# Optimization experiments

Measured on AMD Instinct MI355X. Metric: run time of the kernel, lower is better.

The kernel has to match this reference:

```python
import jax, jax.numpy as jnp
import numpy as np

L_MAX = 16      # max phrase span length in tokens
MARGIN = 0.4    # CosineEmbeddingLoss margin
EPS = 1e-8


def _span_max_pool(sent_emb, sid, start, length):
    """Vectorized ragged span max-pooling.
    sent_emb: [B, S, D]; sid/start/length: [N] int. length in [0, L_MAX-1],
    actual span length = length + 1 (spans are non-empty).
    Returns [N, D].
    """
    offs = jnp.arange(L_MAX, dtype=start.dtype)                  # [L]
    pos = start[:, None] + offs[None, :]                          # [N, L]
    mask = offs[None, :] <= length[:, None]                       # [N, L] (len+1 valid)
    vals = sent_emb[sid[:, None], pos]                            # [N, L, D] gather
    vals = jnp.where(mask[:, :, None], vals, -jnp.inf)
    return jnp.max(vals, axis=1)                                  # [N, D]


def setup_inputs() -> dict:
    key = jax.random.key(0)
    ks = jax.random.split(key, 7)
    B, S, D, N = 64, 512, 1024, 8192
    sent_emb = jax.random.normal(ks[0], (B, S, D), dtype=jnp.float32)
    sid = jax.random.randint(ks[1], (N,), 0, B, dtype=jnp.int32)
    s_start = jax.random.randint(ks[2], (N,), 0, S - L_MAX, dtype=jnp.int32)
    s_len = jax.random.randint(ks[3], (N,), 0, L_MAX, dtype=jnp.int32)
    t_start = jax.random.randint(ks[4], (N,), 0, S - L_MAX, dtype=jnp.int32)
    t_len = jax.random.randint(ks[5], (N,), 0, L_MAX, dtype=jnp.int32)
    labels = jax.random.randint(ks[6], (N,), 0, 2, dtype=jnp.int32)
    return {"sent_emb": sent_emb, "sid": sid, "s_start": s_start, "s_len": s_len,
            "t_start": t_start, "t_len": t_len, "labels": labels}


def reference(sent_emb, sid, s_start, s_len, t_start, t_len, labels):
    # Ragged span max-pooling for source and target phrases
    s_emb = _span_max_pool(sent_emb, sid, s_start, s_len)   # [N, D]
    t_emb = _span_max_pool(sent_emb, sid, t_start, t_len)   # [N, D]
    # CosineEmbeddingLoss (mean reduction), y in {-1, +1}
    dot = jnp.sum(s_emb * t_emb, axis=-1)
    cos = dot / (jnp.linalg.norm(s_emb, axis=-1) * jnp.linalg.norm(t_emb, axis=-1) + EPS)
    y = 2.0 * labels.astype(cos.dtype) - 1.0
    per_pair = jnp.where(y > 0, 1.0 - cos, jnp.maximum(0.0, cos - MARGIN))
    return jnp.mean(per_pair)
```

## Files before the change

### kernel.cpp

```cpp
#include <hip/hip_runtime.h>

#define L_MAX 16
#define MARGIN 0.4f
#define EPS 1e-8f

__global__ __launch_bounds__(256) void span_pair_loss_kernel(
    const float* __restrict__ emb,
    const int*   __restrict__ sid,
    const int*   __restrict__ s_start,
    const int*   __restrict__ s_len,
    const int*   __restrict__ t_start,
    const int*   __restrict__ t_len,
    const int*   __restrict__ labels,
    float*       __restrict__ loss_out,
    int N, int S, int D)
{
    const int wid  = (int)((blockIdx.x * blockDim.x + threadIdx.x) >> 6);
    const int lane = (int)(threadIdx.x & 63);
    if (wid >= N) return;

    const int b = sid[wid];
    const float* __restrict__ base = emb + (size_t)b * (size_t)S * (size_t)D;

    float4 smax[4], tmax[4];

    {
        const int st = s_start[wid];
        const int ln = s_len[wid];
        const float4* __restrict__ row = reinterpret_cast<const float4*>(base + (size_t)st * D);
        const int D4 = D >> 2;
        #pragma unroll
        for (int k = 0; k < 4; ++k)
            smax[k] = row[k * 64 + lane];
        for (int j = 1; j <= ln; ++j) {
            const float4* __restrict__ r = row + (size_t)j * D4;
            #pragma unroll
            for (int k = 0; k < 4; ++k) {
                float4 v = r[k * 64 + lane];
                smax[k].x = fmaxf(smax[k].x, v.x);
                smax[k].y = fmaxf(smax[k].y, v.y);
                smax[k].z = fmaxf(smax[k].z, v.z);
                smax[k].w = fmaxf(smax[k].w, v.w);
            }
        }
    }

    {
        const int st = t_start[wid];
        const int ln = t_len[wid];
        const float4* __restrict__ row = reinterpret_cast<const float4*>(base + (size_t)st * D);
        const int D4 = D >> 2;
        #pragma unroll
        for (int k = 0; k < 4; ++k)
            tmax[k] = row[k * 64 + lane];
        for (int j = 1; j <= ln; ++j) {
            const float4* __restrict__ r = row + (size_t)j * D4;
            #pragma unroll
            for (int k = 0; k < 4; ++k) {
                float4 v = r[k * 64 + lane];
                tmax[k].x = fmaxf(tmax[k].x, v.x);
                tmax[k].y = fmaxf(tmax[k].y, v.y);
                tmax[k].z = fmaxf(tmax[k].z, v.z);
                tmax[k].w = fmaxf(tmax[k].w, v.w);
            }
        }
    }

    float dot = 0.f, ss = 0.f, tt = 0.f;
    #pragma unroll
    for (int k = 0; k < 4; ++k) {
        dot += smax[k].x * tmax[k].x + smax[k].y * tmax[k].y
             + smax[k].z * tmax[k].z + smax[k].w * tmax[k].w;
        ss  += smax[k].x * smax[k].x + smax[k].y * smax[k].y
             + smax[k].z * smax[k].z + smax[k].w * smax[k].w;
        tt  += tmax[k].x * tmax[k].x + tmax[k].y * tmax[k].y
             + tmax[k].z * tmax[k].z + tmax[k].w * tmax[k].w;
    }

    #pragma unroll
    for (int off = 32; off > 0; off >>= 1) {
        dot += __shfl_down(dot, off, 64);
        ss  += __shfl_down(ss,  off, 64);
        tt  += __shfl_down(tt,  off, 64);
    }

    if (lane == 0) {
        float cosv = dot / (sqrtf(ss) * sqrtf(tt) + EPS);
        float l = (labels[wid] > 0) ? (1.0f - cosv)
                                    : fmaxf(0.0f, cosv - MARGIN);
        loss_out[wid] = l;
    }
}

__global__ __launch_bounds__(256) void mean_reduce_kernel(
    const float* __restrict__ loss, float* __restrict__ out, int N)
{
    float sum = 0.f;
    for (int i = (int)threadIdx.x; i < N; i += 256)
        sum += loss[i];
    #pragma unroll
    for (int off = 32; off > 0; off >>= 1)
        sum += __shfl_down(sum, off, 64);

    __shared__ float sdata[4];
    const int w = (int)(threadIdx.x >> 6);
    if ((threadIdx.x & 63) == 0) sdata[w] = sum;
    __syncthreads();
    if (threadIdx.x == 0)
        out[0] = (sdata[0] + sdata[1] + sdata[2] + sdata[3]) / (float)N;
}

extern "C" void kernel_launch(void* const* d_in, const int* in_sizes, int n_in,
                              void* d_out, int out_size, void* d_ws, size_t ws_size,
                              hipStream_t stream) {
    const float* emb     = (const float*)d_in[0];
    const int*   sid     = (const int*)d_in[1];
    const int*   s_start = (const int*)d_in[2];
    const int*   s_len   = (const int*)d_in[3];
    const int*   t_start = (const int*)d_in[4];
    const int*   t_len   = (const int*)d_in[5];
    const int*   labels  = (const int*)d_in[6];

    const int N = in_sizes[1];
    const int S = 512;
    const int D = 1024;

    float* loss_ws = (float*)d_ws;

    const int waves_per_block = 4;
    const int blocks = (N + waves_per_block - 1) / waves_per_block;

    span_pair_loss_kernel<<<blocks, 256, 0, stream>>>(
        emb, sid, s_start, s_len, t_start, t_len, labels, loss_ws, N, S, D);

    mean_reduce_kernel<<<1, 256, 0, stream>>>(loss_ws, (float*)d_out, N);
}
```

Baseline: 253.5 us.

## Sort pairs by sentence and swizzle blocks across XCDs for L2 locality

Adds a histogram/scan kernel and an atomic scatter kernel that build a permutation grouping pairs by sentence id. The main kernel processes pairs in that order, with a block-index swizzle so that consecutive sorted chunks land on the same XCD, so pairs sharing a sentence reuse its rows in the local L2. The source and target span loops are also interleaved so their loads can be in flight together. This costs two extra small launches, a single-block serial histogram over N, and an indirect index load per wave.

```diff
diff --git a/kernel.cpp b/kernel.cpp
--- a/kernel.cpp
+++ b/kernel.cpp
@@ -3,6 +3,34 @@
 #define L_MAX 16
 #define MARGIN 0.4f
 #define EPS 1e-8f
+#define NSENT 64
+
+__global__ __launch_bounds__(256) void hist_scan_kernel(
+    const int* __restrict__ sid, int* __restrict__ cursor, int N)
+{
+    __shared__ int h[NSENT];
+    const int t = (int)threadIdx.x;
+    if (t < NSENT) h[t] = 0;
+    __syncthreads();
+    for (int i = t; i < N; i += 256)
+        atomicAdd(&h[sid[i]], 1);
+    __syncthreads();
+    if (t == 0) {
+        int acc = 0;
+        for (int b = 0; b < NSENT; ++b) { int c = h[b]; cursor[b] = acc; acc += c; }
+    }
+}
+
+__global__ __launch_bounds__(256) void scatter_kernel(
+    const int* __restrict__ sid, int* __restrict__ cursor,
+    int* __restrict__ perm, int N)
+{
+    const int i = (int)(blockIdx.x * 256 + threadIdx.x);
+    if (i < N) {
+        const int p = atomicAdd(&cursor[sid[i]], 1);
+        perm[p] = i;
+    }
+}
 
 __global__ __launch_bounds__(256) void span_pair_loss_kernel(
     const float* __restrict__ emb,
@@ -12,83 +40,86 @@
     const int*   __restrict__ t_start,
     const int*   __restrict__ t_len,
     const int*   __restrict__ labels,
+    const int*   __restrict__ perm,
     float*       __restrict__ loss_out,
     int N, int S, int D)
 {
-    const int wid  = (int)((blockIdx.x * blockDim.x + threadIdx.x) >> 6);
-    const int lane = (int)(threadIdx.x & 63);
-    if (wid >= N) return;
+    const int orig = (int)blockIdx.x;
+    const int nwg  = (int)gridDim.x;
+    const int q = nwg >> 3, r = nwg & 7;
+    const int x = orig & 7, j = orig >> 3;
+    const int swz = (x < r ? x * (q + 1) : r * (q + 1) + (x - r) * q) + j;
 
-    const int b = sid[wid];
+    const int lane  = (int)(threadIdx.x & 63);
+    const int pslot = swz * 4 + (int)(threadIdx.x >> 6);
+    if (pslot >= N) return;
+    const int pid = perm[pslot];
+
+    const int b  = sid[pid];
+    const int ss = s_start[pid];
+    const int ls = s_len[pid];
+    const int ts = t_start[pid];
+    const int lt = t_len[pid];
+
     const float* __restrict__ base = emb + (size_t)b * (size_t)S * (size_t)D;
+    const int D4 = D >> 2;
+    const float4* __restrict__ srow = reinterpret_cast<const float4*>(base + (size_t)ss * D);
+    const float4* __restrict__ trow = reinterpret_cast<const float4*>(base + (size_t)ts * D);
 
-    float4 smax[4], tmax[4];
+    float4 sm[4], tm[4];
+    #pragma unroll
+    for (int k = 0; k < 4; ++k) sm[k] = srow[k * 64 + lane];
+    #pragma unroll
+    for (int k = 0; k < 4; ++k) tm[k] = trow[k * 64 + lane];
 
-    {
-        const int st = s_start[wid];
-        const int ln = s_len[wid];
-        const float4* __restrict__ row = reinterpret_cast<const float4*>(base + (size_t)st * D);
-        const int D4 = D >> 2;
-        #pragma unroll
-        for (int k = 0; k < 4; ++k)
-            smax[k] = row[k * 64 + lane];
-        for (int j = 1; j <= ln; ++j) {
-            const float4* __restrict__ r = row + (size_t)j * D4;
+    const int lmax = max(ls, lt);
+    for (int jj = 1; jj <= lmax; ++jj) {
+        float4 a[4], c[4];
+        const bool ds = (jj <= ls), dt = (jj <= lt);
+        if (ds) {
+            #pragma unroll
+            for (int k = 0; k < 4; ++k) a[k] = srow[(size_t)jj * D4 + k * 64 + lane];
+        }
+        if (dt) {
+            #pragma unroll
+            for (int k = 0; k < 4; ++k) c[k] = trow[(size_t)jj * D4 + k * 64 + lane];
+        }
+        if (ds) {
             #pragma unroll
             for (int k = 0; k < 4; ++k) {
-                float4 v = r[k * 64 + lane];
-                smax[k].x = fmaxf(smax[k].x, v.x);
-                smax[k].y = fmaxf(smax[k].y, v.y);
-                smax[k].z = fmaxf(smax[k].z, v.z);
-                smax[k].w = fmaxf(smax[k].w, v.w);
+                sm[k].x = fmaxf(sm[k].x, a[k].x); sm[k].y = fmaxf(sm[k].y, a[k].y);
+                sm[k].z = fmaxf(sm[k].z, a[k].z); sm[k].w = fmaxf(sm[k].w, a[k].w);
+            }
+        }
+        if (dt) {
+            #pragma unroll
+            for (int k = 0; k < 4; ++k) {
+                tm[k].x = fmaxf(tm[k].x, c[k].x); tm[k].y = fmaxf(tm[k].y, c[k].y);
+                tm[k].z = fmaxf(tm[k].z, c[k].z); tm[k].w = fmaxf(tm[k].w, c[k].w);
             }
         }
     }
 
-    {
-        const int st = t_start[wid];
-        const int ln = t_len[wid];
-        const float4* __restrict__ row = reinterpret_cast<const float4*>(base + (size_t)st * D);
-        const int D4 = D >> 2;
-        #pragma unroll
-        for (int k = 0; k < 4; ++k)
-            tmax[k] = row[k * 64 + lane];
-        for (int j = 1; j <= ln; ++j) {
-            const float4* __restrict__ r = row + (size_t)j * D4;
-            #pragma unroll
-            for (int k = 0; k < 4; ++k) {
-                float4 v = r[k * 64 + lane];
-                tmax[k].x = fmaxf(tmax[k].x, v.x);
-                tmax[k].y = fmaxf(tmax[k].y, v.y);
-                tmax[k].z = fmaxf(tmax[k].z, v.z);
-                tmax[k].w = fmaxf(tmax[k].w, v.w);
-            }
-        }
-    }
-
-    float dot = 0.f, ss = 0.f, tt = 0.f;
+    float dot = 0.f, ssq = 0.f, tsq = 0.f;
     #pragma unroll
     for (int k = 0; k < 4; ++k) {
-        dot += smax[k].x * tmax[k].x + smax[k].y * tmax[k].y
-             + smax[k].z * tmax[k].z + smax[k].w * tmax[k].w;
-        ss  += smax[k].x * smax[k].x + smax[k].y * smax[k].y
-             + smax[k].z * smax[k].z + smax[k].w * smax[k].w;
-        tt  += tmax[k].x * tmax[k].x + tmax[k].y * tmax[k].y
-             + tmax[k].z * tmax[k].z + tmax[k].w * tmax[k].w;
+        dot += sm[k].x * tm[k].x + sm[k].y * tm[k].y + sm[k].z * tm[k].z + sm[k].w * tm[k].w;
+        ssq += sm[k].x * sm[k].x + sm[k].y * sm[k].y + sm[k].z * sm[k].z + sm[k].w * sm[k].w;
+        tsq += tm[k].x * tm[k].x + tm[k].y * tm[k].y + tm[k].z * tm[k].z + tm[k].w * tm[k].w;
     }
 
     #pragma unroll
     for (int off = 32; off > 0; off >>= 1) {
         dot += __shfl_down(dot, off, 64);
-        ss  += __shfl_down(ss,  off, 64);
-        tt  += __shfl_down(tt,  off, 64);
+        ssq += __shfl_down(ssq, off, 64);
+        tsq += __shfl_down(tsq, off, 64);
     }
 
     if (lane == 0) {
-        float cosv = dot / (sqrtf(ss) * sqrtf(tt) + EPS);
-        float l = (labels[wid] > 0) ? (1.0f - cosv)
-                                    : fmaxf(0.0f, cosv - MARGIN);
-        loss_out[wid] = l;
+        const float cosv = dot / (sqrtf(ssq) * sqrtf(tsq) + EPS);
+        const float l = (labels[pid] > 0) ? (1.0f - cosv)
+                                          : fmaxf(0.0f, cosv - MARGIN);
+        loss_out[pid] = l;
     }
 }
 
@@ -126,12 +157,15 @@
     const int D = 1024;
 
     float* loss_ws = (float*)d_ws;
+    int*   perm    = (int*)((char*)d_ws + (size_t)N * 4);
+    int*   cursor  = (int*)((char*)d_ws + (size_t)N * 8);
 
-    const int waves_per_block = 4;
-    const int blocks = (N + waves_per_block - 1) / waves_per_block;
+    hist_scan_kernel<<<1, 256, 0, stream>>>(sid, cursor, N);
+    scatter_kernel<<<(N + 255) / 256, 256, 0, stream>>>(sid, cursor, perm, N);
 
+    const int blocks = (N + 3) / 4;
     span_pair_loss_kernel<<<blocks, 256, 0, stream>>>(
-        emb, sid, s_start, s_len, t_start, t_len, labels, loss_ws, N, S, D);
+        emb, sid, s_start, s_len, t_start, t_len, labels, perm, loss_ws, N, S, D);
 
     mean_reduce_kernel<<<1, 256, 0, stream>>>(loss_ws, (float*)d_out, N);
 }
```

New measurement: 251.6 us. About the same (-0.8%).
